# Optimization experiments

Measured on AMD Instinct MI355X. Metric: run time of the kernel, lower is better.

Reference implementation:

```python
import jax, jax.numpy as jnp
import numpy as np

N = 50000   # nodes
E = 800000  # edges
IN, H1, H2, OUT = 128, 256, 128, 1


def setup_inputs() -> dict:
    key = jax.random.key(0)
    ks = jax.random.split(key, 9)
    x = jax.random.normal(ks[0], (N, IN), dtype=jnp.float32)
    edge_index = jax.random.randint(ks[1], (2, E), 0, N, dtype=jnp.int32)
    def glorot(k, fan_in, fan_out):
        s = np.sqrt(6.0 / (fan_in + fan_out)).astype(np.float32)
        return jax.random.uniform(k, (fan_in, fan_out), jnp.float32, -s, s)
    W1 = glorot(ks[2], IN, H1)
    b1 = jnp.zeros((H1,), jnp.float32)
    W2 = glorot(ks[3], H1, H2)
    b2 = jnp.zeros((H2,), jnp.float32)
    W3 = glorot(ks[4], H2, OUT)
    b3 = jnp.zeros((OUT,), jnp.float32)
    return {"x": x, "edge_index": edge_index, "W1": W1, "b1": b1,
            "W2": W2, "b2": b2, "W3": W3, "b3": b3}


def _gcn_layer(x, W, b, src, dst, norm):
    # dense transform [N, d_in] @ [d_in, d_out]
    h = x @ W
    # degree-normalized sparse aggregation: out[dst] += norm * h[src]
    agg = jax.ops.segment_sum(h[src] * norm[:, None], dst, num_segments=N)
    return agg + b


def reference(x, edge_index, W1, b1, W2, b2, W3, b3):
    src, dst = edge_index[0], edge_index[1]
    # PyG GCNConv: add self loops, then symmetric normalization
    loop = jnp.arange(N, dtype=src.dtype)
    src = jnp.concatenate([src, loop])
    dst = jnp.concatenate([dst, loop])
    deg = jax.ops.segment_sum(jnp.ones_like(dst, jnp.float32), dst, num_segments=N)
    dis = jax.lax.rsqrt(jnp.maximum(deg, 1.0))  # deg >= 1 via self loops
    norm = dis[src] * dis[dst]  # [E+N]
    h1 = jax.nn.relu(_gcn_layer(x, W1, b1, src, dst, norm))
    h2 = jax.nn.relu(_gcn_layer(h1, W2, b2, src, dst, norm))
    y = _gcn_layer(h2, W3, b3, src, dst, norm).reshape(-1)
    return (y, h1, h2)
```

## Files before the change

kernel.cpp:

```cpp
#include <hip/hip_runtime.h>


typedef __attribute__((ext_vector_type(8))) short short8;
typedef __attribute__((ext_vector_type(4))) float f32x4;

static __device__ __forceinline__ unsigned short f2bf(float f){
  union { float f; unsigned u; } v; v.f = f;
  unsigned r = v.u + 0x7FFF + ((v.u >> 16) & 1);
  return (unsigned short)(r >> 16);
}
static __device__ __forceinline__ float2 bf2f2(unsigned u){
  union { unsigned u; float f; } a, b;
  a.u = u << 16; b.u = u & 0xffff0000u;
  return make_float2(a.f, b.f);
}

__global__ __launch_bounds__(256) void k_prepbin(
    const int* __restrict__ src, const int* __restrict__ dst,
    int* __restrict__ bcur, unsigned* __restrict__ pairs, int E, int binB,
    const float* __restrict__ W1, const float* __restrict__ W2,
    unsigned short* __restrict__ Wf1, unsigned short* __restrict__ Wf2){
  __shared__ int cl[256];
  int blk = blockIdx.x;
  int tid = threadIdx.x;
  if (blk < binB){
    int e0 = blk * 4096 + tid;
    cl[tid] = 0; __syncthreads();
    #pragma unroll
    for (int i = 0; i < 16; i++){
      int e = e0 + i*256;
      if (e < E) atomicAdd(&cl[dst[e] >> 8], 1);
    }
    __syncthreads();
    int c = cl[tid];
    int g = (c > 0) ? atomicAdd(&bcur[tid], c) : 0;
    cl[tid] = g;
    __syncthreads();
    #pragma unroll
    for (int i = 0; i < 16; i++){
      int e = e0 + i*256;
      if (e < E){
        int d = dst[e];
        int b = d >> 8;
        int p = atomicAdd(&cl[b], 1);
        pairs[(b << 13) + p] = (unsigned)src[e] | ((unsigned)(d & 255) << 16);
      }
    }
  } else {
    int t = (blk - binB)*256 + tid;
    if (t < 32768){
      int j = t & 7, lane = (t>>3) & 63, kt = (t>>9) & 3, nt = t >> 11;
      int nn = nt*16 + (lane & 15);
      int kk = kt*32 + (lane>>4)*8 + j;
      Wf1[t] = f2bf(W1[kk*256 + nn]);
    } else {
      int o = t - 32768;
      int j = o & 7, lane = (o>>3) & 63, ntl = (o>>9) & 3, kt = (o>>11) & 7, h = o >> 14;
      int nn = (h*4 + ntl)*16 + (lane & 15);
      int kk = kt*32 + (lane>>4)*8 + j;
      Wf2[o] = f2bf(W2[kk*128 + nn]);
    }
  }
}

__global__ __launch_bounds__(256) void k_place(
    const int* __restrict__ bcur, const unsigned* __restrict__ pairs,
    unsigned short* __restrict__ csr_src, int* __restrict__ rowptr,
    int* __restrict__ cnt, float* __restrict__ dis, int n, int nb){
  __shared__ int sh[256];
  __shared__ int ncnt[256];
  int t = threadIdx.x;
  int b = blockIdx.x;
  int v = (t < nb) ? bcur[t] : 0;
  sh[t] = v; __syncthreads();
  for (int off = 1; off < 256; off <<= 1){
    int x = (t >= off) ? sh[t-off] : 0;
    __syncthreads(); sh[t] += x; __syncthreads();
  }
  int csr_base = (b == 0) ? 0 : sh[b-1];
  int cnt_b = bcur[b];
  ncnt[t] = 0; __syncthreads();
  const unsigned* P = pairs + ((size_t)b << 13);
  for (int i = t; i < cnt_b; i += 256) atomicAdd(&ncnt[P[i] >> 16], 1);
  __syncthreads();
  int c = ncnt[t];
  sh[t] = c; __syncthreads();
  for (int off = 1; off < 256; off <<= 1){
    int x = (t >= off) ? sh[t-off] : 0;
    __syncthreads(); sh[t] += x; __syncthreads();
  }
  int noff = sh[t] - c;
  int node = (b << 8) + t;
  if (node < n){
    rowptr[node] = csr_base + noff;
    cnt[node] = c;
    dis[node] = rsqrtf((float)(c + 1));
  }
  ncnt[t] = noff; __syncthreads();
  for (int i = t; i < cnt_b; i += 256){
    unsigned u = P[i];
    int p = atomicAdd(&ncnt[u >> 16], 1);
    csr_src[csr_base + p] = (unsigned short)(u & 0xffff);
  }
}

__global__ __launch_bounds__(256) void k_xscale(
    const float4* __restrict__ x, const float* __restrict__ dis,
    uint2* __restrict__ xbs, int n){
  int i = blockIdx.x*256 + threadIdx.x;
  if (i >= n*32) return;
  float d = dis[i >> 5];
  float4 v = x[i];
  xbs[i] = make_uint2((unsigned)f2bf(d*v.x) | ((unsigned)f2bf(d*v.y) << 16),
                      (unsigned)f2bf(d*v.z) | ((unsigned)f2bf(d*v.w) << 16));
}

__global__ void k_aggL1(const unsigned* __restrict__ xbs, unsigned* __restrict__ out,
                        const int* __restrict__ rowptr, const int* __restrict__ cnt,
                        const unsigned short* __restrict__ csr_src,
                        const float* __restrict__ dis, int n){
  int t = threadIdx.x;
  int lane = t & 63;
  int node = blockIdx.x*4 + (t >> 6);
  if (node >= n) return;
  float di = dis[node];
  float2 acc = bf2f2(xbs[(size_t)node*64 + lane]);
  int start = rowptr[node];
  int mm = cnt[node];
  int j = 0;
  for (; j + 15 < mm; j += 16){
    int s[16]; unsigned uv[16];
    #pragma unroll
    for (int q = 0; q < 16; q++) s[q] = csr_src[start+j+q];
    #pragma unroll
    for (int q = 0; q < 16; q++) uv[q] = xbs[(size_t)s[q]*64 + lane];
    #pragma unroll
    for (int q = 0; q < 16; q++){
      float2 u = bf2f2(uv[q]);
      acc.x += u.x; acc.y += u.y;
    }
  }
  for (; j + 3 < mm; j += 4){
    int s[4]; unsigned uv[4];
    #pragma unroll
    for (int q = 0; q < 4; q++) s[q] = csr_src[start+j+q];
    #pragma unroll
    for (int q = 0; q < 4; q++) uv[q] = xbs[(size_t)s[q]*64 + lane];
    #pragma unroll
    for (int q = 0; q < 4; q++){
      float2 u = bf2f2(uv[q]);
      acc.x += u.x; acc.y += u.y;
    }
  }
  for (; j < mm; j++){
    float2 u = bf2f2(xbs[(size_t)csr_src[start+j]*64 + lane]);
    acc.x += u.x; acc.y += u.y;
  }
  out[(size_t)node*64 + lane] =
      (unsigned)f2bf(di*acc.x) | ((unsigned)f2bf(di*acc.y) << 16);
}

__global__ void k_aggL2(const unsigned* __restrict__ t2s, float* __restrict__ h2,
                        const int* __restrict__ rowptr, const int* __restrict__ cnt,
                        const unsigned short* __restrict__ csr_src,
                        const float* __restrict__ dis,
                        const float* __restrict__ b2, const float* __restrict__ W3,
                        float* __restrict__ u, int n){
  int t = threadIdx.x;
  int lane = t & 63;
  int node = blockIdx.x*4 + (t >> 6);
  if (node >= n) return;
  float di = dis[node];
  float2 acc = bf2f2(t2s[(size_t)node*64 + lane]);
  int start = rowptr[node];
  int mm = cnt[node];
  int j = 0;
  for (; j + 15 < mm; j += 16){
    int s[16]; unsigned uv[16];
    #pragma unroll
    for (int q = 0; q < 16; q++) s[q] = csr_src[start+j+q];
    #pragma unroll
    for (int q = 0; q < 16; q++) uv[q] = t2s[(size_t)s[q]*64 + lane];
    #pragma unroll
    for (int q = 0; q < 16; q++){
      float2 uu = bf2f2(uv[q]);
      acc.x += uu.x; acc.y += uu.y;
    }
  }
  for (; j + 3 < mm; j += 4){
    int s[4]; unsigned uv[4];
    #pragma unroll
    for (int q = 0; q < 4; q++) s[q] = csr_src[start+j+q];
    #pragma unroll
    for (int q = 0; q < 4; q++) uv[q] = t2s[(size_t)s[q]*64 + lane];
    #pragma unroll
    for (int q = 0; q < 4; q++){
      float2 uu = bf2f2(uv[q]);
      acc.x += uu.x; acc.y += uu.y;
    }
  }
  for (; j < mm; j++){
    float2 uu = bf2f2(t2s[(size_t)csr_src[start+j]*64 + lane]);
    acc.x += uu.x; acc.y += uu.y;
  }
  float2 b = ((const float2*)b2)[lane];
  acc.x = fmaxf(fmaf(di, acc.x, b.x), 0.0f);
  acc.y = fmaxf(fmaf(di, acc.y, b.y), 0.0f);
  ((float2*)h2)[(size_t)node*64 + lane] = acc;
  float up = fmaf(acc.x, W3[2*lane], acc.y * W3[2*lane+1]);
  #pragma unroll
  for (int off = 32; off > 0; off >>= 1) up += __shfl_down(up, off);
  if (lane == 0) u[node] = di * up;
}

__global__ __launch_bounds__(256) void k_gemm1_mfma(
    const unsigned short* __restrict__ Xa, const unsigned short* __restrict__ Wf1,
    const float* __restrict__ bias, float* __restrict__ out, int n)
{
  __shared__ unsigned short Wl[8*4*64*8];
  int t = threadIdx.x;
  int row0 = (blockIdx.x >> 1) * 64;
  int h = blockIdx.x & 1;
  int w = t >> 6, lane = t & 63, m = lane & 15, q = lane >> 4;
  int rbase = w*16;
  int rowm = row0 + rbase + m;
  int ra = (rowm < n) ? rowm : (n-1);
  const short8* Arow = (const short8*)(Xa + (size_t)ra*128);
  short8 af[4];
  #pragma unroll
  for (int kt = 0; kt < 4; kt++) af[kt] = Arow[kt*4 + q];
  {
    const float4* src = (const float4*)Wf1 + (size_t)h*2048;
    float4* dst = (float4*)Wl;
    #pragma unroll
    for (int i = 0; i < 8; i++) dst[i*256 + t] = src[i*256 + t];
  }
  __syncthreads();
  f32x4 acc[8];
  #pragma unroll
  for (int i = 0; i < 8; i++) acc[i] = (f32x4){0.f,0.f,0.f,0.f};
  const short8* Wv = (const short8*)Wl;
  #pragma unroll
  for (int nt = 0; nt < 8; nt++){
    #pragma unroll
    for (int kt = 0; kt < 4; kt++){
      short8 bfr = Wv[(nt*4 + kt)*64 + lane];
      acc[nt] = __builtin_amdgcn_mfma_f32_16x16x32_bf16(af[kt], bfr, acc[nt], 0, 0, 0);
    }
  }
  int rowa = row0 + rbase + q*4;
  int colb = h*128 + m;
  #pragma unroll
  for (int nt = 0; nt < 8; nt++){
    float b = bias[colb + nt*16];
    #pragma unroll
    for (int r = 0; r < 4; r++){
      int rr = rowa + r;
      if (rr < n)
        out[(size_t)rr*256 + colb + nt*16] = fmaxf(acc[nt][r] + b, 0.0f);
    }
  }
}

__global__ __launch_bounds__(256) void k_gemm2_mfma(
    const float* __restrict__ H1, const unsigned short* __restrict__ Wf2,
    const float* __restrict__ dis, unsigned short* __restrict__ T2s, int n)
{
  __shared__ unsigned short Wl[32*64*8];
  int t = threadIdx.x;
  int row0 = (blockIdx.x >> 1) * 64;
  int h = blockIdx.x & 1;
  int w = t >> 6, lane = t & 63, m = lane & 15, q = lane >> 4;
  int rbase = w*16;
  int rowm = row0 + rbase + m;
  int ra = (rowm < n) ? rowm : (n-1);
  const float4* Arow = (const float4*)(H1 + (size_t)ra*256);
  short8 af[8];
  #pragma unroll
  for (int kt = 0; kt < 8; kt++){
    float4 a0 = Arow[kt*8 + q*2];
    float4 a1 = Arow[kt*8 + q*2 + 1];
    short8 v;
    v[0] = (short)f2bf(a0.x); v[1] = (short)f2bf(a0.y);
    v[2] = (short)f2bf(a0.z); v[3] = (short)f2bf(a0.w);
    v[4] = (short)f2bf(a1.x); v[5] = (short)f2bf(a1.y);
    v[6] = (short)f2bf(a1.z); v[7] = (short)f2bf(a1.w);
    af[kt] = v;
  }
  {
    const float4* src = (const float4*)Wf2 + (size_t)h*2048;
    float4* dst = (float4*)Wl;
    #pragma unroll
    for (int i = 0; i < 8; i++) dst[i*256 + t] = src[i*256 + t];
  }
  __syncthreads();
  f32x4 acc[4];
  #pragma unroll
  for (int i = 0; i < 4; i++) acc[i] = (f32x4){0.f,0.f,0.f,0.f};
  const short8* Wv = (const short8*)Wl;
  #pragma unroll
  for (int nt = 0; nt < 4; nt++){
    #pragma unroll
    for (int kt = 0; kt < 8; kt++){
      short8 bfr = Wv[(kt*4 + nt)*64 + lane];
      acc[nt] = __builtin_amdgcn_mfma_f32_16x16x32_bf16(af[kt], bfr, acc[nt], 0, 0, 0);
    }
  }
  int rowa = row0 + rbase + q*4;
  float dsv[4];
  #pragma unroll
  for (int r = 0; r < 4; r++){
    int rr = rowa + r;
    dsv[r] = (rr < n) ? dis[rr] : 0.0f;
  }
  #pragma unroll
  for (int nt = 0; nt < 4; nt++){
    int col = h*64 + nt*16 + m;
    #pragma unroll
    for (int r = 0; r < 4; r++){
      int rr = rowa + r;
      if (rr < n) T2s[(size_t)rr*128 + col] = f2bf(dsv[r] * acc[nt][r]);
    }
  }
}

__global__ void k_agg1d(const float* __restrict__ us, float* __restrict__ y,
                        const int* __restrict__ rowptr, const int* __restrict__ cnt,
                        const unsigned short* __restrict__ csr_src,
                        const float* __restrict__ dis,
                        const float* __restrict__ b3, int n){
  int t = threadIdx.x;
  int node = blockIdx.x*16 + (t >> 4);
  int sub = t & 15;
  if (node >= n) return;
  int s0 = rowptr[node];
  int m = cnt[node];
  float acc = (sub == 0) ? us[node] : 0.0f;
  for (int j = sub; j < m; j += 16)
    acc += us[csr_src[s0 + j]];
  #pragma unroll
  for (int off = 8; off > 0; off >>= 1) acc += __shfl_xor(acc, off);
  if (sub == 0) y[node] = fmaf(dis[node], acc, b3[0]);
}

extern "C" void kernel_launch(void* const* d_in, const int* in_sizes, int n_in,
                              void* d_out, int out_size, void* d_ws, size_t ws_size,
                              hipStream_t stream){
  const float* x  = (const float*)d_in[0];
  const int*  ei  = (const int*)d_in[1];
  const float* W1 = (const float*)d_in[2];
  const float* b1 = (const float*)d_in[3];
  const float* W2 = (const float*)d_in[4];
  const float* b2 = (const float*)d_in[5];
  const float* W3 = (const float*)d_in[6];
  const float* b3 = (const float*)d_in[7];
  const int N = in_sizes[0] / 128;
  const int E = in_sizes[1] / 2;
  const int* src = ei;
  const int* dst = ei + E;
  const int NB = (N + 255) >> 8;

  char* p = (char*)d_ws;
  auto alloc = [&](size_t bytes)->char*{
    char* r = p; p += (bytes + 255) & ~(size_t)255; return r;
  };
  int*   bcur    = (int*)  alloc(256*4);
  int*   rowptr  = (int*)  alloc((size_t)N*4);
  int*   cnt     = (int*)  alloc((size_t)N*4);
  float* dis     = (float*)alloc((size_t)N*4);
  unsigned* pairs = (unsigned*)alloc((size_t)NB*8192*4);
  unsigned short* csr_src = (unsigned short*)alloc((size_t)E*2);
  unsigned* xbs  = (unsigned*)alloc((size_t)N*128*2);
  unsigned* xa   = (unsigned*)alloc((size_t)N*128*2);
  unsigned short* t2s = (unsigned short*)alloc((size_t)N*128*2);
  float* u       = (float*)alloc((size_t)N*4);
  unsigned short* wf1 = (unsigned short*)alloc(32768*2);
  unsigned short* wf2 = (unsigned short*)alloc(32768*2);

  float* y  = (float*)d_out;
  float* h1 = y + N;
  float* h2 = h1 + (size_t)N*256;

  int bb = (E + 4095)/4096;

  hipMemsetAsync(bcur, 0, 256*4, stream);
  k_prepbin <<<bb + 256, 256, 0, stream>>>(
      src, dst, bcur, pairs, E, bb, W1, W2, wf1, wf2);
  k_place   <<<NB, 256, 0, stream>>>(bcur, pairs, csr_src, rowptr, cnt, dis, N, NB);

  int xq = N*32;
  k_xscale  <<<(xq + 255)/256, 256, 0, stream>>>((const float4*)x, dis, (uint2*)xbs, N);

  int ab = (N + 3)/4;
  int rb = (N + 63)/64;
  k_aggL1     <<<ab,   256, 0, stream>>>(xbs, xa, rowptr, cnt, csr_src, dis, N);
  k_gemm1_mfma<<<rb*2, 256, 0, stream>>>((const unsigned short*)xa, wf1, b1, h1, N);
  k_gemm2_mfma<<<rb*2, 256, 0, stream>>>(h1, wf2, dis, t2s, N);
  k_aggL2     <<<ab,   256, 0, stream>>>((const unsigned*)t2s, h2, rowptr, cnt, csr_src, dis, b2, W3, u, N);
  k_agg1d     <<<(N + 15)/16, 256, 0, stream>>>(u, y, rowptr, cnt, csr_src, dis, b3, N);
}
```

Before: 253.4 us.

## Fuse layer-1 aggregation with both GEMMs and fold x scaling into placement

The x prescale/bf16 cast moves into k_place, reusing the per-node dis values held in shared memory. A new k_fused1 kernel aggregates 64 nodes into swizzled LDS, then runs the W1 GEMM and the W2 GEMM in the same block. This removes the xa intermediate buffer and three kernel launches. In exchange, each 512-thread block holds about 144 KB of LDS (both weight matrices plus the activation tile), which limits occupancy to one block per CU during the latency-bound gather. Every block also reloads the full weights from global memory.

```diff
diff --git a/kernel.cpp b/kernel.cpp
--- a/kernel.cpp
+++ b/kernel.cpp
@@ -66,16 +66,19 @@
 __global__ __launch_bounds__(256) void k_place(
     const int* __restrict__ bcur, const unsigned* __restrict__ pairs,
     unsigned short* __restrict__ csr_src, int* __restrict__ rowptr,
-    int* __restrict__ cnt, float* __restrict__ dis, int n, int nb){
+    int* __restrict__ cnt, float* __restrict__ dis,
+    const float4* __restrict__ x, uint2* __restrict__ xbs,
+    int n, int nb){
   __shared__ int sh[256];
   __shared__ int ncnt[256];
+  __shared__ float disl[256];
   int t = threadIdx.x;
   int b = blockIdx.x;
   int v = (t < nb) ? bcur[t] : 0;
   sh[t] = v; __syncthreads();
   for (int off = 1; off < 256; off <<= 1){
-    int x = (t >= off) ? sh[t-off] : 0;
-    __syncthreads(); sh[t] += x; __syncthreads();
+    int xx = (t >= off) ? sh[t-off] : 0;
+    __syncthreads(); sh[t] += xx; __syncthreads();
   }
   int csr_base = (b == 0) ? 0 : sh[b-1];
   int cnt_b = bcur[b];
@@ -86,15 +89,17 @@
   int c = ncnt[t];
   sh[t] = c; __syncthreads();
   for (int off = 1; off < 256; off <<= 1){
-    int x = (t >= off) ? sh[t-off] : 0;
-    __syncthreads(); sh[t] += x; __syncthreads();
+    int xx = (t >= off) ? sh[t-off] : 0;
+    __syncthreads(); sh[t] += xx; __syncthreads();
   }
   int noff = sh[t] - c;
   int node = (b << 8) + t;
+  float di = rsqrtf((float)(c + 1));
+  disl[t] = di;
   if (node < n){
     rowptr[node] = csr_base + noff;
     cnt[node] = c;
-    dis[node] = rsqrtf((float)(c + 1));
+    dis[node] = di;
   }
   ncnt[t] = noff; __syncthreads();
   for (int i = t; i < cnt_b; i += 256){
@@ -102,62 +107,171 @@
     int p = atomicAdd(&ncnt[u >> 16], 1);
     csr_src[csr_base + p] = (unsigned short)(u & 0xffff);
   }
-}
-
-__global__ __launch_bounds__(256) void k_xscale(
-    const float4* __restrict__ x, const float* __restrict__ dis,
-    uint2* __restrict__ xbs, int n){
-  int i = blockIdx.x*256 + threadIdx.x;
-  if (i >= n*32) return;
-  float d = dis[i >> 5];
-  float4 v = x[i];
-  xbs[i] = make_uint2((unsigned)f2bf(d*v.x) | ((unsigned)f2bf(d*v.y) << 16),
-                      (unsigned)f2bf(d*v.z) | ((unsigned)f2bf(d*v.w) << 16));
-}
-
-__global__ void k_aggL1(const unsigned* __restrict__ xbs, unsigned* __restrict__ out,
-                        const int* __restrict__ rowptr, const int* __restrict__ cnt,
-                        const unsigned short* __restrict__ csr_src,
-                        const float* __restrict__ dis, int n){
+  const float4* xg = x + (size_t)b*8192;
+  uint2* xo = xbs + (size_t)b*8192;
+  int lim = n*32 - b*8192;
+  for (int i = t; i < 8192 && i < lim; i += 256){
+    float d = disl[i >> 5];
+    float4 vv = xg[i];
+    xo[i] = make_uint2((unsigned)f2bf(d*vv.x) | ((unsigned)f2bf(d*vv.y) << 16),
+                       (unsigned)f2bf(d*vv.z) | ((unsigned)f2bf(d*vv.w) << 16));
+  }
+}
+
+__global__ __launch_bounds__(512) void k_fused1(
+    const unsigned* __restrict__ xbs,
+    const int* __restrict__ rowptr, const int* __restrict__ cnt,
+    const unsigned short* __restrict__ csr_src,
+    const float* __restrict__ dis,
+    const unsigned short* __restrict__ Wf1, const unsigned short* __restrict__ Wf2,
+    const float* __restrict__ b1,
+    float* __restrict__ h1, unsigned short* __restrict__ T2s, int n)
+{
+  __shared__ unsigned short W1l[32768];
+  __shared__ unsigned short W2l[32768];
+  __shared__ unsigned short xal[8192];
   int t = threadIdx.x;
-  int lane = t & 63;
-  int node = blockIdx.x*4 + (t >> 6);
-  if (node >= n) return;
-  float di = dis[node];
-  float2 acc = bf2f2(xbs[(size_t)node*64 + lane]);
-  int start = rowptr[node];
-  int mm = cnt[node];
-  int j = 0;
-  for (; j + 15 < mm; j += 16){
-    int s[16]; unsigned uv[16];
-    #pragma unroll
-    for (int q = 0; q < 16; q++) s[q] = csr_src[start+j+q];
-    #pragma unroll
-    for (int q = 0; q < 16; q++) uv[q] = xbs[(size_t)s[q]*64 + lane];
-    #pragma unroll
-    for (int q = 0; q < 16; q++){
-      float2 u = bf2f2(uv[q]);
-      acc.x += u.x; acc.y += u.y;
-    }
-  }
-  for (; j + 3 < mm; j += 4){
-    int s[4]; unsigned uv[4];
-    #pragma unroll
-    for (int q = 0; q < 4; q++) s[q] = csr_src[start+j+q];
-    #pragma unroll
-    for (int q = 0; q < 4; q++) uv[q] = xbs[(size_t)s[q]*64 + lane];
-    #pragma unroll
-    for (int q = 0; q < 4; q++){
-      float2 u = bf2f2(uv[q]);
-      acc.x += u.x; acc.y += u.y;
-    }
-  }
-  for (; j < mm; j++){
-    float2 u = bf2f2(xbs[(size_t)csr_src[start+j]*64 + lane]);
-    acc.x += u.x; acc.y += u.y;
-  }
-  out[(size_t)node*64 + lane] =
-      (unsigned)f2bf(di*acc.x) | ((unsigned)f2bf(di*acc.y) << 16);
+  int w = t >> 6, lane = t & 63;
+  int row0 = blockIdx.x * 64;
+
+  {
+    const float4* s1 = (const float4*)Wf1;  float4* d1 = (float4*)W1l;
+    const float4* s2 = (const float4*)Wf2;  float4* d2 = (float4*)W2l;
+    #pragma unroll
+    for (int i = 0; i < 8; i++) d1[i*512 + t] = s1[i*512 + t];
+    #pragma unroll
+    for (int i = 0; i < 8; i++) d2[i*512 + t] = s2[i*512 + t];
+  }
+
+  for (int k = 0; k < 8; k++){
+    int nloc = w*8 + k;
+    int node = row0 + nloc;
+    float2 acc = make_float2(0.f, 0.f);
+    if (node < n){
+      acc = bf2f2(xbs[(size_t)node*64 + lane]);
+      int start = rowptr[node];
+      int mm = cnt[node];
+      int j = 0;
+      for (; j + 15 < mm; j += 16){
+        int s[16]; unsigned uv[16];
+        #pragma unroll
+        for (int q = 0; q < 16; q++) s[q] = csr_src[start+j+q];
+        #pragma unroll
+        for (int q = 0; q < 16; q++) uv[q] = xbs[(size_t)s[q]*64 + lane];
+        #pragma unroll
+        for (int q = 0; q < 16; q++){
+          float2 u = bf2f2(uv[q]);
+          acc.x += u.x; acc.y += u.y;
+        }
+      }
+      for (; j + 3 < mm; j += 4){
+        int s[4]; unsigned uv[4];
+        #pragma unroll
+        for (int q = 0; q < 4; q++) s[q] = csr_src[start+j+q];
+        #pragma unroll
+        for (int q = 0; q < 4; q++) uv[q] = xbs[(size_t)s[q]*64 + lane];
+        #pragma unroll
+        for (int q = 0; q < 4; q++){
+          float2 u = bf2f2(uv[q]);
+          acc.x += u.x; acc.y += u.y;
+        }
+      }
+      for (; j < mm; j++){
+        float2 u = bf2f2(xbs[(size_t)csr_src[start+j]*64 + lane]);
+        acc.x += u.x; acc.y += u.y;
+      }
+      float di = dis[node];
+      acc.x *= di; acc.y *= di;
+    }
+    unsigned off = (unsigned)(lane*4) ^ ((unsigned)(nloc & 7) << 4);
+    *(unsigned*)((char*)xal + nloc*256 + off) =
+        (unsigned)f2bf(acc.x) | ((unsigned)f2bf(acc.y) << 16);
+  }
+  __syncthreads();
+
+  int m = lane & 15, q = lane >> 4;
+  int stripe = w & 3;
+  int nth = w >> 2;
+  short8 af[4];
+  {
+    int rl = stripe*16 + m;
+    #pragma unroll
+    for (int kt = 0; kt < 4; kt++){
+      unsigned off = (unsigned)(kt*64 + q*16) ^ ((unsigned)(rl & 7) << 4);
+      af[kt] = *(const short8*)((const char*)xal + rl*256 + off);
+    }
+  }
+  f32x4 acc1[8];
+  #pragma unroll
+  for (int i = 0; i < 8; i++) acc1[i] = (f32x4){0.f,0.f,0.f,0.f};
+  const short8* Wv1 = (const short8*)W1l;
+  #pragma unroll
+  for (int nt = 0; nt < 8; nt++){
+    int ntg = nth*8 + nt;
+    #pragma unroll
+    for (int kt = 0; kt < 4; kt++){
+      short8 bfr = Wv1[(ntg*4 + kt)*64 + lane];
+      acc1[nt] = __builtin_amdgcn_mfma_f32_16x16x32_bf16(af[kt], bfr, acc1[nt], 0, 0, 0);
+    }
+  }
+  int rowa = row0 + stripe*16 + q*4;
+  #pragma unroll
+  for (int nt = 0; nt < 8; nt++){
+    int col = nth*128 + nt*16 + m;
+    float b = b1[col];
+    #pragma unroll
+    for (int r = 0; r < 4; r++){
+      int rr = rowa + r;
+      if (rr < n)
+        h1[(size_t)rr*256 + col] = fmaxf(acc1[nt][r] + b, 0.0f);
+    }
+  }
+  __syncthreads();
+
+  short8 af2[8];
+  {
+    int rowm = row0 + stripe*16 + m;
+    int ra = (rowm < n) ? rowm : (n-1);
+    const float4* A2 = (const float4*)(h1 + (size_t)ra*256);
+    #pragma unroll
+    for (int kt = 0; kt < 8; kt++){
+      float4 a0 = A2[kt*8 + q*2];
+      float4 a1 = A2[kt*8 + q*2 + 1];
+      short8 vv;
+      vv[0] = (short)f2bf(a0.x); vv[1] = (short)f2bf(a0.y);
+      vv[2] = (short)f2bf(a0.z); vv[3] = (short)f2bf(a0.w);
+      vv[4] = (short)f2bf(a1.x); vv[5] = (short)f2bf(a1.y);
+      vv[6] = (short)f2bf(a1.z); vv[7] = (short)f2bf(a1.w);
+      af2[kt] = vv;
+    }
+  }
+  f32x4 acc2[4];
+  #pragma unroll
+  for (int i = 0; i < 4; i++) acc2[i] = (f32x4){0.f,0.f,0.f,0.f};
+  const short8* Wv2 = (const short8*)W2l;
+  #pragma unroll
+  for (int nt = 0; nt < 4; nt++){
+    #pragma unroll
+    for (int kt = 0; kt < 8; kt++){
+      short8 bfr = Wv2[((nth*8 + kt)*4 + nt)*64 + lane];
+      acc2[nt] = __builtin_amdgcn_mfma_f32_16x16x32_bf16(af2[kt], bfr, acc2[nt], 0, 0, 0);
+    }
+  }
+  float dsv[4];
+  #pragma unroll
+  for (int r = 0; r < 4; r++){
+    int rr = rowa + r;
+    dsv[r] = (rr < n) ? dis[rr] : 0.0f;
+  }
+  #pragma unroll
+  for (int nt = 0; nt < 4; nt++){
+    int col = nth*64 + nt*16 + m;
+    #pragma unroll
+    for (int r = 0; r < 4; r++){
+      int rr = rowa + r;
+      if (rr < n) T2s[(size_t)rr*128 + col] = f2bf(dsv[r] * acc2[nt][r]);
+    }
+  }
 }
 
 __global__ void k_aggL2(const unsigned* __restrict__ t2s, float* __restrict__ h2,
@@ -213,117 +327,6 @@
   if (lane == 0) u[node] = di * up;
 }
 
-__global__ __launch_bounds__(256) void k_gemm1_mfma(
-    const unsigned short* __restrict__ Xa, const unsigned short* __restrict__ Wf1,
-    const float* __restrict__ bias, float* __restrict__ out, int n)
-{
-  __shared__ unsigned short Wl[8*4*64*8];
-  int t = threadIdx.x;
-  int row0 = (blockIdx.x >> 1) * 64;
-  int h = blockIdx.x & 1;
-  int w = t >> 6, lane = t & 63, m = lane & 15, q = lane >> 4;
-  int rbase = w*16;
-  int rowm = row0 + rbase + m;
-  int ra = (rowm < n) ? rowm : (n-1);
-  const short8* Arow = (const short8*)(Xa + (size_t)ra*128);
-  short8 af[4];
-  #pragma unroll
-  for (int kt = 0; kt < 4; kt++) af[kt] = Arow[kt*4 + q];
-  {
-    const float4* src = (const float4*)Wf1 + (size_t)h*2048;
-    float4* dst = (float4*)Wl;
-    #pragma unroll
-    for (int i = 0; i < 8; i++) dst[i*256 + t] = src[i*256 + t];
-  }
-  __syncthreads();
-  f32x4 acc[8];
-  #pragma unroll
-  for (int i = 0; i < 8; i++) acc[i] = (f32x4){0.f,0.f,0.f,0.f};
-  const short8* Wv = (const short8*)Wl;
-  #pragma unroll
-  for (int nt = 0; nt < 8; nt++){
-    #pragma unroll
-    for (int kt = 0; kt < 4; kt++){
-      short8 bfr = Wv[(nt*4 + kt)*64 + lane];
-      acc[nt] = __builtin_amdgcn_mfma_f32_16x16x32_bf16(af[kt], bfr, acc[nt], 0, 0, 0);
-    }
-  }
-  int rowa = row0 + rbase + q*4;
-  int colb = h*128 + m;
-  #pragma unroll
-  for (int nt = 0; nt < 8; nt++){
-    float b = bias[colb + nt*16];
-    #pragma unroll
-    for (int r = 0; r < 4; r++){
-      int rr = rowa + r;
-      if (rr < n)
-        out[(size_t)rr*256 + colb + nt*16] = fmaxf(acc[nt][r] + b, 0.0f);
-    }
-  }
-}
-
-__global__ __launch_bounds__(256) void k_gemm2_mfma(
-    const float* __restrict__ H1, const unsigned short* __restrict__ Wf2,
-    const float* __restrict__ dis, unsigned short* __restrict__ T2s, int n)
-{
-  __shared__ unsigned short Wl[32*64*8];
-  int t = threadIdx.x;
-  int row0 = (blockIdx.x >> 1) * 64;
-  int h = blockIdx.x & 1;
-  int w = t >> 6, lane = t & 63, m = lane & 15, q = lane >> 4;
-  int rbase = w*16;
-  int rowm = row0 + rbase + m;
-  int ra = (rowm < n) ? rowm : (n-1);
-  const float4* Arow = (const float4*)(H1 + (size_t)ra*256);
-  short8 af[8];
-  #pragma unroll
-  for (int kt = 0; kt < 8; kt++){
-    float4 a0 = Arow[kt*8 + q*2];
-    float4 a1 = Arow[kt*8 + q*2 + 1];
-    short8 v;
-    v[0] = (short)f2bf(a0.x); v[1] = (short)f2bf(a0.y);
-    v[2] = (short)f2bf(a0.z); v[3] = (short)f2bf(a0.w);
-    v[4] = (short)f2bf(a1.x); v[5] = (short)f2bf(a1.y);
-    v[6] = (short)f2bf(a1.z); v[7] = (short)f2bf(a1.w);
-    af[kt] = v;
-  }
-  {
-    const float4* src = (const float4*)Wf2 + (size_t)h*2048;
-    float4* dst = (float4*)Wl;
-    #pragma unroll
-    for (int i = 0; i < 8; i++) dst[i*256 + t] = src[i*256 + t];
-  }
-  __syncthreads();
-  f32x4 acc[4];
-  #pragma unroll
-  for (int i = 0; i < 4; i++) acc[i] = (f32x4){0.f,0.f,0.f,0.f};
-  const short8* Wv = (const short8*)Wl;
-  #pragma unroll
-  for (int nt = 0; nt < 4; nt++){
-    #pragma unroll
-    for (int kt = 0; kt < 8; kt++){
-      short8 bfr = Wv[(kt*4 + nt)*64 + lane];
-      acc[nt] = __builtin_amdgcn_mfma_f32_16x16x32_bf16(af[kt], bfr, acc[nt], 0, 0, 0);
-    }
-  }
-  int rowa = row0 + rbase + q*4;
-  float dsv[4];
-  #pragma unroll
-  for (int r = 0; r < 4; r++){
-    int rr = rowa + r;
-    dsv[r] = (rr < n) ? dis[rr] : 0.0f;
-  }
-  #pragma unroll
-  for (int nt = 0; nt < 4; nt++){
-    int col = h*64 + nt*16 + m;
-    #pragma unroll
-    for (int r = 0; r < 4; r++){
-      int rr = rowa + r;
-      if (rr < n) T2s[(size_t)rr*128 + col] = f2bf(dsv[r] * acc[nt][r]);
-    }
-  }
-}
-
 __global__ void k_agg1d(const float* __restrict__ us, float* __restrict__ y,
                         const int* __restrict__ rowptr, const int* __restrict__ cnt,
                         const unsigned short* __restrict__ csr_src,
@@ -371,7 +374,6 @@
   unsigned* pairs = (unsigned*)alloc((size_t)NB*8192*4);
   unsigned short* csr_src = (unsigned short*)alloc((size_t)E*2);
   unsigned* xbs  = (unsigned*)alloc((size_t)N*128*2);
-  unsigned* xa   = (unsigned*)alloc((size_t)N*128*2);
   unsigned short* t2s = (unsigned short*)alloc((size_t)N*128*2);
   float* u       = (float*)alloc((size_t)N*4);
   unsigned short* wf1 = (unsigned short*)alloc(32768*2);
@@ -386,16 +388,15 @@
   hipMemsetAsync(bcur, 0, 256*4, stream);
   k_prepbin <<<bb + 256, 256, 0, stream>>>(
       src, dst, bcur, pairs, E, bb, W1, W2, wf1, wf2);
-  k_place   <<<NB, 256, 0, stream>>>(bcur, pairs, csr_src, rowptr, cnt, dis, N, NB);
-
-  int xq = N*32;
-  k_xscale  <<<(xq + 255)/256, 256, 0, stream>>>((const float4*)x, dis, (uint2*)xbs, N);
+  k_place   <<<NB, 256, 0, stream>>>(bcur, pairs, csr_src, rowptr, cnt, dis,
+                                     (const float4*)x, (uint2*)xbs, N, NB);
+
+  int rb = (N + 63)/64;
+  k_fused1  <<<rb, 512, 0, stream>>>(xbs, rowptr, cnt, csr_src, dis,
+                                     wf1, wf2, b1, h1, t2s, N);
 
   int ab = (N + 3)/4;
-  int rb = (N + 63)/64;
-  k_aggL1     <<<ab,   256, 0, stream>>>(xbs, xa, rowptr, cnt, csr_src, dis, N);
-  k_gemm1_mfma<<<rb*2, 256, 0, stream>>>((const unsigned short*)xa, wf1, b1, h1, N);
-  k_gemm2_mfma<<<rb*2, 256, 0, stream>>>(h1, wf2, dis, t2s, N);
-  k_aggL2     <<<ab,   256, 0, stream>>>((const unsigned*)t2s, h2, rowptr, cnt, csr_src, dis, b2, W3, u, N);
-  k_agg1d     <<<(N + 15)/16, 256, 0, stream>>>(u, y, rowptr, cnt, csr_src, dis, b3, N);
-}
+  k_aggL2   <<<ab, 256, 0, stream>>>((const unsigned*)t2s, h2, rowptr, cnt,
+                                     csr_src, dis, b2, W3, u, N);
+  k_agg1d   <<<(N + 15)/16, 256, 0, stream>>>(u, y, rowptr, cnt, csr_src, dis, b3, N);
+}
```

After: 325.3 us. 1.28x slower.
